# Optimization experiments

Measured on AMD Instinct MI355X. Metric: run time of the kernel, lower is better.

Reference implementation:

```python
import jax, jax.numpy as jnp
import numpy as np

N = 100000   # nodes
H = 96       # hidden_dim
A = 32       # attn_dim
De = 16      # edge_embeddings_dim
E = 500000   # edges per edge type
NEG_SLOPE = 0.01  # torch F.leaky_relu default


def setup_inputs() -> dict:
    key = jax.random.key(0)
    ks = jax.random.split(key, 24)
    nrm = lambda k, shape, s=1.0: jax.random.normal(k, shape, dtype=jnp.float32) * s
    idx = lambda k: jax.random.randint(k, (E,), 0, N, dtype=jnp.int32)
    Din = 2 * H + De
    return {
        'h': nrm(ks[0], (N, H)),
        'src0': idx(ks[1]), 'dst0': idx(ks[2]),
        'src1': idx(ks[3]), 'dst1': idx(ks[4]),
        'src2': idx(ks[5]), 'dst2': idx(ks[6]),
        'Wm0': nrm(ks[7], (Din, H), Din ** -0.5), 'bm0': jnp.zeros((H,), jnp.float32), 'ef0': nrm(ks[8], (De,)),
        'Wm1': nrm(ks[9], (Din, H), Din ** -0.5), 'bm1': jnp.zeros((H,), jnp.float32), 'ef1': nrm(ks[10], (De,)),
        'Wm2': nrm(ks[11], (Din, H), Din ** -0.5), 'bm2': jnp.zeros((H,), jnp.float32), 'ef2': nrm(ks[12], (De,)),
        'Wn0': nrm(ks[13], (H, A), H ** -0.5), 'Wa0': nrm(ks[14], (2 * A, 1), (2 * A) ** -0.5),
        'Wn1': nrm(ks[15], (H, A), H ** -0.5), 'Wa1': nrm(ks[16], (2 * A, 1), (2 * A) ** -0.5),
        'Wu': nrm(ks[17], (4 * H, H), (4 * H) ** -0.5), 'bu': jnp.zeros((H,), jnp.float32),
    }


def _leaky(x):
    return jnp.where(x > 0, x, NEG_SLOPE * x)


def _edge_msg(h, src, dst, Wm, bm, ef):
    # cat(src_h, dst_h, edge_feature) -> Linear  (dropout p=0, eval mode)
    x = jnp.concatenate([h[src], h[dst], jnp.broadcast_to(ef, (src.shape[0], ef.shape[0]))], axis=-1)
    return x @ Wm + bm  # [E, H]


def _mean_agg(m, dst):
    # fn.mean('m','msg'): per-destination mean over incoming edges
    s = jax.ops.segment_sum(m, dst, num_segments=N)
    c = jax.ops.segment_sum(jnp.ones((m.shape[0],), m.dtype), dst, num_segments=N)
    return s / jnp.maximum(c, 1.0)[:, None]


def _attn_agg(scores, m, dst):
    # per-destination softmax over mailbox (variable-size), then weighted sum
    smax = jax.ops.segment_max(scores, dst, num_segments=N)
    ex = jnp.exp(scores - smax[dst])
    den = jax.ops.segment_sum(ex, dst, num_segments=N)
    num = jax.ops.segment_sum(ex[:, None] * m, dst, num_segments=N)
    return num / jnp.maximum(den, 1e-9)[:, None]


def reference(h, src0, dst0, src1, dst1, src2, dst2,
              Wm0, bm0, ef0, Wm1, bm1, ef1, Wm2, bm2, ef2,
              Wn0, Wa0, Wn1, Wa1, Wu, bu):
    # edge type 0: intra_diff (attention), type 1: inter_diff (attention), type 2: intra_lt (mean)
    m0 = _edge_msg(h, src0, dst0, Wm0, bm0, ef0)
    m1 = _edge_msg(h, src1, dst1, Wm1, bm1, ef1)
    m2 = _edge_msg(h, src2, dst2, Wm2, bm2, ef2)

    z0 = h @ Wn0  # [N, A]
    s0 = _leaky(jnp.concatenate([z0[src0], z0[dst0]], axis=-1) @ Wa0)[:, 0]  # [E]
    z1 = h @ Wn1
    s1 = _leaky(jnp.concatenate([z1[src1], z1[dst1]], axis=-1) @ Wa1)[:, 0]

    msg0 = _attn_agg(s0, m0, dst0)   # [N, H]
    msg1 = _attn_agg(s1, m1, dst1)
    msg2 = _mean_agg(m2, dst2)

    # cross_reducer='stack' then concat over edge-type dim -> [N, 3H]
    mcat = jnp.concatenate([msg0, msg1, msg2], axis=-1)
    # cell node update: Linear(cat(h, m)) + ReLU
    return jax.nn.relu(jnp.concatenate([h, mcat], axis=-1) @ Wu + bu)
```

## Files before the change

kernel.cpp:

```cpp
#include <hip/hip_runtime.h>
#include <hip/hip_bf16.h>
#include <cstdint>

#define NN 100000
#define HH 96
#define AD 32
#define DE 16
#define EE 500000
#define NEG 0.01f

#define GSH 9
#define GSZ 512
#define KB 196
#define CH 2048
#define BPT 245
#define PCAP 801056

#define PREP_B 128
#define CAST_B 12500
#define HIST_B 512

typedef __bf16 bf16x8 __attribute__((ext_vector_type(8)));
typedef float  f32x4  __attribute__((ext_vector_type(4)));
typedef unsigned long long ull;
typedef unsigned long long ull2 __attribute__((ext_vector_type(2)));

__device__ __forceinline__ unsigned short f2b(float x) {
    union { float f; unsigned int u; } v; v.f = x;
    unsigned int r = v.u + 0x7fffu + ((v.u >> 16) & 1u);
    return (unsigned short)(r >> 16);
}
__device__ __forceinline__ float b2f(unsigned short h) {
    union { unsigned int u; float f; } v; v.u = ((unsigned int)h) << 16;
    return v.f;
}

__global__ __launch_bounds__(256) void setup_kernel(
    const float* __restrict__ h,
    const float* Wm0, const float* bm0, const float* ef0,
    const float* Wm1, const float* bm1, const float* ef1,
    const float* Wm2, const float* bm2, const float* ef2,
    const float* Wn0, const float* Wa0,
    const float* Wn1, const float* Wa1,
    const float* Wu,
    const int* __restrict__ d0, const int* __restrict__ d1,
    const int* __restrict__ d2,
    float* cvec, float* wvec,
    unsigned short* BfN, unsigned short* BfU,
    unsigned short* __restrict__ hb, float* __restrict__ uv,
    int* __restrict__ bCnt) {
    __shared__ int hist[3 * KB];
    int bid = blockIdx.x;
    int t = threadIdx.x;
    if (bid < PREP_B) {
        const float* Wm[3] = {Wm0, Wm1, Wm2};
        const float* bm[3] = {bm0, bm1, bm2};
        const float* ef[3] = {ef0, ef1, ef2};
        const int total = 288 + 384 + 55296 + 36864;
        for (int i = bid * 256 + t; i < total; i += PREP_B * 256) {
            if (i < 288) {
                int ty = i / 96, j = i % 96;
                float s = bm[ty][j];
                for (int k = 0; k < DE; ++k) s += ef[ty][k] * Wm[ty][(2 * HH + k) * HH + j];
                cvec[i] = s;
            } else if (i < 288 + 384) {
                int ii = i - 288;
                int kind = ii / 96, k = ii % 96;
                const float* Wn = (kind < 2) ? Wn0 : Wn1;
                const float* Wa = (kind < 2) ? Wa0 : Wa1;
                int off = (kind & 1) ? AD : 0;
                float s = 0.f;
                for (int a = 0; a < AD; ++a) s += Wn[k * AD + a] * Wa[off + a];
                wvec[ii] = s;
            } else if (i < 288 + 384 + 55296) {
                int ii = i - 672;
                int sec = ii / 9216; int rem = ii % 9216;
                int ksc = rem / 512; int lj = rem % 512;
                int ks = ksc / 6, c = ksc % 6;
                int lane = lj / 8, jj = lj % 8;
                int quad = lane / 16, m = lane % 16;
                int k = ks * 32 + quad * 8 + jj;
                int n = c * 16 + m;
                int mt = (sec < 3) ? sec : sec - 3;
                int rowoff = (sec < 3) ? 0 : HH;
                BfN[ii] = f2b(Wm[mt][(rowoff + k) * HH + n]);
            } else {
                int ii = i - (672 + 55296);
                int ksc = ii / 512; int lj = ii % 512;
                int ks = ksc / 6, c = ksc % 6;
                int lane = lj / 8, jj = lj % 8;
                int quad = lane / 16, m = lane % 16;
                int k = ks * 32 + quad * 8 + jj;
                int n = c * 16 + m;
                BfU[ii] = f2b(Wu[k * HH + n]);
            }
        }
    } else if (bid < PREP_B + CAST_B) {
        int lane = t & 31;
        int node = (((bid - PREP_B) * 256 + t) >> 5);
        if (node >= NN) return;
        float h0 = h[node * HH + lane];
        float h1 = h[node * HH + 32 + lane];
        float h2 = h[node * HH + 64 + lane];
        hb[node * HH + lane] = f2b(h0);
        hb[node * HH + 32 + lane] = f2b(h1);
        hb[node * HH + 64 + lane] = f2b(h2);
        float acc[4];
#pragma unroll
        for (int q = 0; q < 4; ++q)
            acc[q] = h0 * wvec[q * 96 + lane] + h1 * wvec[q * 96 + 32 + lane] +
                     h2 * wvec[q * 96 + 64 + lane];
#pragma unroll
        for (int d = 16; d >= 1; d >>= 1)
#pragma unroll
            for (int q = 0; q < 4; ++q) acc[q] += __shfl_down(acc[q], d, 32);
        if (lane == 0) {
#pragma unroll
            for (int q = 0; q < 4; ++q) uv[q * NN + node] = acc[q];
        }
    } else {
        int hb_ = bid - (PREP_B + CAST_B);
        for (int j = t; j < 3 * KB; j += 256) hist[j] = 0;
        __syncthreads();
        const int total = 3 * EE;
        for (int i = hb_ * 256 + t; i < total; i += HIST_B * 256) {
            int ty = i / EE, e = i - ty * EE;
            const int* d = (ty == 0) ? d0 : (ty == 1) ? d1 : d2;
            atomicAdd(&hist[ty * KB + (d[e] >> GSH)], 1);
        }
        __syncthreads();
        for (int j = t; j < 3 * KB; j += 256)
            if (hist[j]) atomicAdd(&bCnt[j], hist[j]);
    }
}

__global__ void cast_uv_fix_kernel(const float* __restrict__ h,
                                   const float* __restrict__ Wn0, const float* __restrict__ Wa0,
                                   const float* __restrict__ Wn1, const float* __restrict__ Wa1,
                                   float* __restrict__ uv) {
}

__global__ void bucket_scan(const int* __restrict__ bCnt, int* __restrict__ bBase,
                            int* __restrict__ gCursor) {
    __shared__ int hist[3 * KB];
    int t = threadIdx.x;
    if (t < 3 * KB) hist[t] = bCnt[t];
    __syncthreads();
    if (t < 3) {
        int run = 0;
        for (int b = 0; b < KB; ++b) {
            bBase[t * (KB + 1) + b] = run;
            gCursor[t * KB + b] = run;
            run += hist[t * KB + b];
        }
        bBase[t * (KB + 1) + KB] = run;
    }
}

__global__ __launch_bounds__(256) void bucket_scatter(
    const int* __restrict__ s0, const int* __restrict__ d0,
    const int* __restrict__ s1, const int* __restrict__ d1,
    const int* __restrict__ s2, const int* __restrict__ d2,
    int* __restrict__ gCursor, unsigned int* __restrict__ binned) {
    __shared__ unsigned int recs[CH];
    __shared__ unsigned short rnk[CH];
    __shared__ unsigned char bkt[CH];
    __shared__ int cnt[KB];
    __shared__ int gpos[KB];
    int t = threadIdx.x;
    int type = blockIdx.x / BPT;
    int chunk = (blockIdx.x % BPT) * CH;
    const int* src = (type == 0) ? s0 : (type == 1) ? s1 : s2;
    const int* dst = (type == 0) ? d0 : (type == 1) ? d1 : d2;
    if (t < KB) cnt[t] = 0;
    __syncthreads();
#pragma unroll
    for (int k = 0; k < CH / 256; ++k) {
        int idx = k * 256 + t;
        int e = chunk + idx;
        if (e < EE) {
            int s = src[e], d = dst[e];
            int b = d >> GSH;
            recs[idx] = ((unsigned int)s << GSH) | (unsigned int)(d & (GSZ - 1));
            bkt[idx] = (unsigned char)b;
            rnk[idx] = (unsigned short)atomicAdd(&cnt[b], 1);
        } else {
            bkt[idx] = 0xFF;
        }
    }
    __syncthreads();
    if (t < KB) {
        int c = cnt[t];
        gpos[t] = (c > 0) ? atomicAdd(&gCursor[type * KB + t], c) : 0;
    }
    __syncthreads();
    unsigned int* bout = binned + (size_t)type * EE;
#pragma unroll
    for (int k = 0; k < CH / 256; ++k) {
        int idx = k * 256 + t;
        unsigned char b = bkt[idx];
        if (b != 0xFF) bout[gpos[b] + rnk[idx]] = recs[idx];
    }
}

__global__ __launch_bounds__(256) void bucket_sort(
    const unsigned int* __restrict__ binned, const int* __restrict__ bBase,
    const float* __restrict__ uv,
    ull* __restrict__ rse, ull* __restrict__ wrec) {
    __shared__ int cnt[GSZ];
    __shared__ float vbuf[GSZ];
    __shared__ int wsum[4];
    int t = threadIdx.x;
    int type = blockIdx.x / KB;
    int b = blockIdx.x % KB;
    int nodeBase = b * GSZ;
    int eb = bBase[type * (KB + 1) + b];
    int en = bBase[type * (KB + 1) + b + 1];
    int n = en - eb;
    int pbase = eb + 3 * GSZ * b;
    const unsigned int* bin = binned + (size_t)type * EE + eb;
    cnt[t] = 0;
    cnt[t + 256] = 0;
    if (type < 2) {
        const float* vsrc = uv + (2 * type + 1) * NN;
        int nd0 = nodeBase + t, nd1 = nodeBase + 256 + t;
        vbuf[t] = (nd0 < NN) ? vsrc[nd0] : 0.f;
        vbuf[t + 256] = (nd1 < NN) ? vsrc[nd1] : 0.f;
    }
    __syncthreads();
    for (int i = t; i < n; i += 256) atomicAdd(&cnt[bin[i] & (GSZ - 1)], 1);
    __syncthreads();
    int v0 = cnt[t * 2], v1 = cnt[t * 2 + 1];
    int p0 = (v0 + 3) & ~3, p1 = (v1 + 3) & ~3;
    int s = p0 + p1;
    int lane = t & 63, wv = t >> 6;
    int val = s;
#pragma unroll
    for (int d = 1; d < 64; d <<= 1) {
        int o = __shfl_up(val, d, 64);
        if (lane >= d) val += o;
    }
    if (lane == 63) wsum[wv] = val;
    __syncthreads();
    int wpre = 0;
#pragma unroll
    for (int i = 0; i < 4; ++i) wpre += (i < wv) ? wsum[i] : 0;
    int excl = val - s + wpre;
    int off0 = excl, off1 = excl + p0;
    ull* wb = wrec + (size_t)type * PCAP;
    int node0 = nodeBase + t * 2, node1 = nodeBase + t * 2 + 1;
    if (node0 < NN) {
        rse[(size_t)type * NN + node0] =
            ((ull)(unsigned int)p0 << 32) | (unsigned int)(pbase + off0);
        for (int q = v0; q < p0; ++q) wb[pbase + off0 + q] = 0ull;
    }
    if (node1 < NN) {
        rse[(size_t)type * NN + node1] =
            ((ull)(unsigned int)p1 << 32) | (unsigned int)(pbase + off1);
        for (int q = v1; q < p1; ++q) wb[pbase + off1 + q] = 0ull;
    }
    __syncthreads();
    cnt[t * 2] = off0;
    cnt[t * 2 + 1] = off1;
    __syncthreads();
    const float* usrc = uv + 2 * type * NN;
    for (int i = t; i < n; i += 256) {
        unsigned int r = bin[i];
        int dl = r & (GSZ - 1);
        int p = atomicAdd(&cnt[dl], 1);
        unsigned int sidx = r >> GSH;
        float w = 1.f;
        if (type < 2) {
            float c = usrc[sidx] + vbuf[dl];
            c = fmaxf(c, NEG * c);
            w = __expf(c);
        }
        wb[pbase + p] = ((ull)__float_as_uint(w) << 32) | (ull)(sidx * 192u);
    }
}

__global__ void aggregate_kernel(const ull* __restrict__ rse,
                                 const ull* __restrict__ wrec,
                                 const unsigned short* __restrict__ hb,
                                 unsigned short* __restrict__ hagg,
                                 float* __restrict__ den) {
    const size_t NH = (size_t)NN * HH;
    int lane = threadIdx.x & 31;
    int node = (blockIdx.x * blockDim.x + threadIdx.x) >> 5;
    if (node >= NN) return;
    int t = blockIdx.y;
    ull se = rse[(size_t)t * NN + node];
    int beg = (int)(unsigned int)se;
    int end = beg + (int)(se >> 32);
    const ull* wr = wrec + (size_t)t * PCAP;
    float a0 = 0.f, a1 = 0.f, a2 = 0.f, dn = 0.f;
    const char* b0 = (const char*)hb + 4 * lane;
    const char* b1 = (const char*)hb + 128 + 2 * lane;
#define EDGE(rec)                                                              \
    {                                                                          \
        float w = __uint_as_float((unsigned int)((rec) >> 32));                \
        unsigned int off = (unsigned int)(rec);                                \
        unsigned int dv = *(const unsigned int*)(b0 + off);                    \
        unsigned int sv = *(const unsigned short*)(b1 + off);                  \
        a0 += w * __uint_as_float(dv << 16);                                   \
        a1 += w * __uint_as_float(dv & 0xFFFF0000u);                           \
        a2 += w * __uint_as_float(sv << 16);                                   \
        dn += w;                                                               \
    }
    for (int j = beg; j < end; j += 4) {
        ull2 p0 = *(const ull2*)(wr + j);
        ull2 p1 = *(const ull2*)(wr + j + 2);
        EDGE(p0[0]);
        EDGE(p0[1]);
        EDGE(p1[0]);
        EDGE(p1[1]);
    }
#undef EDGE
    float inv = (dn > 0.f) ? 1.f / dn : 0.f;
    float q0 = a0 * inv, q1 = a1 * inv, q2 = a2 * inv;
    char* mr = (char*)(hagg + (size_t)t * NH + (size_t)node * HH);
    *(unsigned int*)(mr + 4 * lane) =
        (unsigned int)f2b(q0) | ((unsigned int)f2b(q1) << 16);
    *(unsigned short*)(mr + 128 + 2 * lane) = f2b(q2);
    if (lane == 0) den[(size_t)t * NN + node] = dn;
}

__global__ __launch_bounds__(256) void msg_gemm_kernel(const unsigned short* __restrict__ hagg,
                                                       const unsigned short* __restrict__ hb,
                                                       const unsigned short* __restrict__ BfN,
                                                       const float* __restrict__ den,
                                                       const float* __restrict__ cvec,
                                                       unsigned short* __restrict__ msgb) {
    const size_t NH = (size_t)NN * HH;
    int wave = threadIdx.x >> 6;
    int lane = threadIdx.x & 63;
    int quad = lane >> 4, m = lane & 15;
    int blk = blockIdx.x * 4 + wave;
    if (blk >= NN / 16) return;
    int r0 = blk * 16;
    bf16x8 hf[3];
#pragma unroll
    for (int ks = 0; ks < 3; ++ks)
        hf[ks] = *(const bf16x8*)(hb + (size_t)(r0 + m) * HH + ks * 32 + quad * 8);
    for (int t = 0; t < 3; ++t) {
        const unsigned short* ha = hagg + (size_t)t * NH;
        f32x4 acc[6] = {};
#pragma unroll
        for (int ks = 0; ks < 3; ++ks) {
            bf16x8 af = *(const bf16x8*)(ha + (size_t)(r0 + m) * HH + ks * 32 + quad * 8);
#pragma unroll
            for (int c = 0; c < 6; ++c) {
                bf16x8 bfv = *(const bf16x8*)(BfN + (((t * 3 + ks) * 6 + c) << 9) + lane * 8);
                acc[c] = __builtin_amdgcn_mfma_f32_16x16x32_bf16(af, bfv, acc[c], 0, 0, 0);
            }
        }
#pragma unroll
        for (int ks = 0; ks < 3; ++ks) {
#pragma unroll
            for (int c = 0; c < 6; ++c) {
                bf16x8 bfv = *(const bf16x8*)(BfN + ((((t + 3) * 3 + ks) * 6 + c) << 9) + lane * 8);
                acc[c] = __builtin_amdgcn_mfma_f32_16x16x32_bf16(hf[ks], bfv, acc[c], 0, 0, 0);
            }
        }
        float dn[4];
#pragma unroll
        for (int r = 0; r < 4; ++r) dn[r] = den[(size_t)t * NN + r0 + quad * 4 + r];
#pragma unroll
        for (int c = 0; c < 6; ++c) {
            float cv = cvec[t * 96 + c * 16 + m];
#pragma unroll
            for (int r = 0; r < 4; ++r) {
                int row = r0 + quad * 4 + r;
                float val = (dn[r] > 0.f) ? (acc[c][r] + cv) : 0.f;
                msgb[(size_t)row * 288 + t * 96 + c * 16 + m] = f2b(val);
            }
        }
    }
}

__global__ __launch_bounds__(256) void update_gemm_kernel(const unsigned short* __restrict__ hb,
                                                          const unsigned short* __restrict__ msgb,
                                                          const unsigned short* __restrict__ BfU,
                                                          const float* __restrict__ bu,
                                                          float* __restrict__ out) {
    int wave = threadIdx.x >> 6;
    int lane = threadIdx.x & 63;
    int quad = lane >> 4, m = lane & 15;
    int blk = blockIdx.x * 4 + wave;
    if (blk >= NN / 16) return;
    int r0 = blk * 16;
    f32x4 acc[6] = {};
#pragma unroll
    for (int ks = 0; ks < 12; ++ks) {
        const unsigned short* ap =
            (ks < 3) ? hb + (size_t)(r0 + m) * HH + ks * 32 + quad * 8
                     : msgb + (size_t)(r0 + m) * 288 + (ks - 3) * 32 + quad * 8;
        bf16x8 af = *(const bf16x8*)ap;
#pragma unroll
        for (int c = 0; c < 6; ++c) {
            bf16x8 bfv = *(const bf16x8*)(BfU + ((ks * 6 + c) << 9) + lane * 8);
            acc[c] = __builtin_amdgcn_mfma_f32_16x16x32_bf16(af, bfv, acc[c], 0, 0, 0);
        }
    }
#pragma unroll
    for (int c = 0; c < 6; ++c) {
        float b = bu[c * 16 + m];
#pragma unroll
        for (int r = 0; r < 4; ++r) {
            int row = r0 + quad * 4 + r;
            float v2 = acc[c][r] + b;
            out[(size_t)row * HH + c * 16 + m] = v2 > 0.f ? v2 : 0.f;
        }
    }
}

extern "C" void kernel_launch(void* const* d_in, const int* in_sizes, int n_in,
                              void* d_out, int out_size, void* d_ws, size_t ws_size,
                              hipStream_t stream) {
    (void)in_sizes; (void)n_in; (void)out_size;
    const float* h   = (const float*)d_in[0];
    const int* srcs[3] = {(const int*)d_in[1], (const int*)d_in[3], (const int*)d_in[5]};
    const int* dsts[3] = {(const int*)d_in[2], (const int*)d_in[4], (const int*)d_in[6]};
    const float* Wm0 = (const float*)d_in[7];
    const float* bm0 = (const float*)d_in[8];
    const float* ef0 = (const float*)d_in[9];
    const float* Wm1 = (const float*)d_in[10];
    const float* bm1 = (const float*)d_in[11];
    const float* ef1 = (const float*)d_in[12];
    const float* Wm2 = (const float*)d_in[13];
    const float* bm2 = (const float*)d_in[14];
    const float* ef2 = (const float*)d_in[15];
    const float* Wn0 = (const float*)d_in[16];
    const float* Wa0 = (const float*)d_in[17];
    const float* Wn1 = (const float*)d_in[18];
    const float* Wa1 = (const float*)d_in[19];
    const float* Wu  = (const float*)d_in[20];
    const float* bu  = (const float*)d_in[21];
    float* out = (float*)d_out;

    const size_t NEED = 165019776;
    if (ws_size < NEED) return;
    char* w = (char*)d_ws;
    unsigned short* msgb    = (unsigned short*)(w + 0);
    unsigned short* hb      = (unsigned short*)(w + 57600000);
    unsigned short* hagg    = (unsigned short*)(w + 76800000);
    float*          den     = (float*)(w + 134400000);
    float*          uv      = (float*)(w + 135600000);
    float*          cvec    = (float*)(w + 137200000);
    float*          wvec    = (float*)(w + 137201280);
    unsigned short* BfN     = (unsigned short*)(w + 137202816);
    unsigned short* BfU     = (unsigned short*)(w + 137313408);
    int*            bBase   = (int*)(w + 137387136);
    int*            gCursor = (int*)(w + 137389568);
    int*            bCnt    = (int*)(w + 137392000);
    ull*            rse     = (ull*)(w + 137394432);
    unsigned int*   binned  = (unsigned int*)(w + 139794432);
    ull*            wrec    = (ull*)(w + 145794432);

    hipMemsetAsync(bCnt, 0, 3 * KB * sizeof(int), stream);
    {
        struct L {
            static __global__ void k(const float* Wn0, const float* Wa0,
                                     const float* Wn1, const float* Wa1,
                                     float* wvec) {
                int ii = blockIdx.x * 192 + threadIdx.x;
                if (ii >= 384) return;
                int kind = ii / 96, kk = ii % 96;
                const float* Wn = (kind < 2) ? Wn0 : Wn1;
                const float* Wa = (kind < 2) ? Wa0 : Wa1;
                int off = (kind & 1) ? AD : 0;
                float s = 0.f;
                for (int a = 0; a < AD; ++a) s += Wn[kk * AD + a] * Wa[off + a];
                wvec[ii] = s;
            }
        };
        L::k<<<2, 192, 0, stream>>>(Wn0, Wa0, Wn1, Wa1, wvec);
    }
    setup_kernel<<<PREP_B + CAST_B + HIST_B, 256, 0, stream>>>(
        h, Wm0, bm0, ef0, Wm1, bm1, ef1, Wm2, bm2, ef2,
        Wn0, Wa0, Wn1, Wa1, Wu, dsts[0], dsts[1], dsts[2],
        cvec, wvec, BfN, BfU, hb, uv, bCnt);
    bucket_scan<<<1, 640, 0, stream>>>(bCnt, bBase, gCursor);
    bucket_scatter<<<3 * BPT, 256, 0, stream>>>(srcs[0], dsts[0], srcs[1], dsts[1],
                                                srcs[2], dsts[2], gCursor, binned);
    bucket_sort<<<3 * KB, 256, 0, stream>>>(binned, bBase, uv, rse, wrec);

    aggregate_kernel<<<dim3(12500, 3), 256, 0, stream>>>(rse, wrec, hb, hagg, den);
    msg_gemm_kernel<<<1563, 256, 0, stream>>>(hagg, hb, BfN, den, cvec, msgb);
    update_gemm_kernel<<<1563, 256, 0, stream>>>(hb, msgb, BfU, bu, out);
}
```

Before: 327.4 us.

## Fold message linear into update weights and fuse the two output GEMMs

Precomputes combined weights Wm·Wu so the per-edge-type message projection and the node-update GEMM run as one 384-wide GEMM directly on aggregated features. This removes the intermediate bf16 message buffer and a whole kernel. Nodes with no incoming edges of some type get their spurious constant and dst-term contributions subtracted in a new fixup kernel using a stored correction matrix. The trade-off is heavier serial weight precompute in setup, with per-thread 96-long dot products, plus an extra pass over the output. The folded bf16 weights may also lose some precision.

```diff
diff --git a/kernel.cpp b/kernel.cpp
--- a/kernel.cpp
+++ b/kernel.cpp
@@ -40,13 +40,11 @@
     const float* Wm0, const float* bm0, const float* ef0,
     const float* Wm1, const float* bm1, const float* ef1,
     const float* Wm2, const float* bm2, const float* ef2,
-    const float* Wn0, const float* Wa0,
-    const float* Wn1, const float* Wa1,
     const float* Wu,
     const int* __restrict__ d0, const int* __restrict__ d1,
     const int* __restrict__ d2,
-    float* cvec, float* wvec,
-    unsigned short* BfN, unsigned short* BfU,
+    const float* __restrict__ wvec,
+    unsigned short* BfF, float* Dmat, float* cb,
     unsigned short* __restrict__ hb, float* __restrict__ uv,
     int* __restrict__ bCnt) {
     __shared__ int hist[3 * KB];
@@ -56,43 +54,55 @@
         const float* Wm[3] = {Wm0, Wm1, Wm2};
         const float* bm[3] = {bm0, bm1, bm2};
         const float* ef[3] = {ef0, ef1, ef2};
-        const int total = 288 + 384 + 55296 + 36864;
+        const int T_BFF = 36864, T_D = 27648, T_CB = 288;
+        const int total = T_BFF + T_D + T_CB;
         for (int i = bid * 256 + t; i < total; i += PREP_B * 256) {
-            if (i < 288) {
-                int ty = i / 96, j = i % 96;
-                float s = bm[ty][j];
-                for (int k = 0; k < DE; ++k) s += ef[ty][k] * Wm[ty][(2 * HH + k) * HH + j];
-                cvec[i] = s;
-            } else if (i < 288 + 384) {
-                int ii = i - 288;
-                int kind = ii / 96, k = ii % 96;
-                const float* Wn = (kind < 2) ? Wn0 : Wn1;
-                const float* Wa = (kind < 2) ? Wa0 : Wa1;
-                int off = (kind & 1) ? AD : 0;
-                float s = 0.f;
-                for (int a = 0; a < AD; ++a) s += Wn[k * AD + a] * Wa[off + a];
-                wvec[ii] = s;
-            } else if (i < 288 + 384 + 55296) {
-                int ii = i - 672;
-                int sec = ii / 9216; int rem = ii % 9216;
-                int ksc = rem / 512; int lj = rem % 512;
+            if (i < T_BFF) {
+                int ksc = i / 512, lj = i % 512;
                 int ks = ksc / 6, c = ksc % 6;
                 int lane = lj / 8, jj = lj % 8;
                 int quad = lane / 16, m = lane % 16;
                 int k = ks * 32 + quad * 8 + jj;
                 int n = c * 16 + m;
-                int mt = (sec < 3) ? sec : sec - 3;
-                int rowoff = (sec < 3) ? 0 : HH;
-                BfN[ii] = f2b(Wm[mt][(rowoff + k) * HH + n]);
+                float s;
+                if (k < 96) {
+                    s = Wu[k * HH + n];
+                    for (int tt = 0; tt < 3; ++tt) {
+                        const float* wm = Wm[tt];
+                        float a = 0.f;
+                        for (int j = 0; j < 96; ++j)
+                            a += wm[(96 + k) * HH + j] * Wu[(96 + 96 * tt + j) * HH + n];
+                        s += a;
+                    }
+                } else {
+                    int tt = (k - 96) / 96, kk = (k - 96) % 96;
+                    const float* wm = Wm[tt];
+                    s = 0.f;
+                    for (int j = 0; j < 96; ++j)
+                        s += wm[kk * HH + j] * Wu[(96 + 96 * tt + j) * HH + n];
+                }
+                BfF[i] = f2b(s);
+            } else if (i < T_BFF + T_D) {
+                int ii = i - T_BFF;
+                int tt = ii / 9216, r = ii % 9216;
+                int k = r / 96, n = r % 96;
+                const float* wm = Wm[tt];
+                float s = 0.f;
+                for (int j = 0; j < 96; ++j)
+                    s += wm[(96 + k) * HH + j] * Wu[(96 + 96 * tt + j) * HH + n];
+                Dmat[ii] = s;
             } else {
-                int ii = i - (672 + 55296);
-                int ksc = ii / 512; int lj = ii % 512;
-                int ks = ksc / 6, c = ksc % 6;
-                int lane = lj / 8, jj = lj % 8;
-                int quad = lane / 16, m = lane % 16;
-                int k = ks * 32 + quad * 8 + jj;
-                int n = c * 16 + m;
-                BfU[ii] = f2b(Wu[k * HH + n]);
+                int ii = i - T_BFF - T_D;
+                int tt = ii / 96, n = ii % 96;
+                const float* wm = Wm[tt];
+                float s = 0.f;
+                for (int k = 0; k < 96; ++k) {
+                    float cv = bm[tt][k];
+                    for (int j = 0; j < DE; ++j)
+                        cv += ef[tt][j] * wm[(192 + j) * HH + k];
+                    s += cv * Wu[(96 + 96 * tt + k) * HH + n];
+                }
+                cb[ii] = s;
             }
         }
     } else if (bid < PREP_B + CAST_B) {
@@ -132,12 +142,6 @@
         for (int j = t; j < 3 * KB; j += 256)
             if (hist[j]) atomicAdd(&bCnt[j], hist[j]);
     }
-}
-
-__global__ void cast_uv_fix_kernel(const float* __restrict__ h,
-                                   const float* __restrict__ Wn0, const float* __restrict__ Wa0,
-                                   const float* __restrict__ Wn1, const float* __restrict__ Wa1,
-                                   float* __restrict__ uv) {
 }
 
 __global__ void bucket_scan(const int* __restrict__ bCnt, int* __restrict__ bBase,
@@ -325,12 +329,14 @@
     if (lane == 0) den[(size_t)t * NN + node] = dn;
 }
 
-__global__ __launch_bounds__(256) void msg_gemm_kernel(const unsigned short* __restrict__ hagg,
-                                                       const unsigned short* __restrict__ hb,
-                                                       const unsigned short* __restrict__ BfN,
-                                                       const float* __restrict__ den,
-                                                       const float* __restrict__ cvec,
-                                                       unsigned short* __restrict__ msgb) {
+__global__ __launch_bounds__(256) void fused_out_kernel(
+    const unsigned short* __restrict__ hagg,
+    const unsigned short* __restrict__ hb,
+    const unsigned short* __restrict__ BfF,
+    const float* __restrict__ den,
+    const float* __restrict__ cb,
+    const float* __restrict__ bu,
+    float* __restrict__ out) {
     const size_t NH = (size_t)NN * HH;
     int wave = threadIdx.x >> 6;
     int lane = threadIdx.x & 63;
@@ -338,79 +344,80 @@
     int blk = blockIdx.x * 4 + wave;
     if (blk >= NN / 16) return;
     int r0 = blk * 16;
-    bf16x8 hf[3];
-#pragma unroll
-    for (int ks = 0; ks < 3; ++ks)
-        hf[ks] = *(const bf16x8*)(hb + (size_t)(r0 + m) * HH + ks * 32 + quad * 8);
-    for (int t = 0; t < 3; ++t) {
-        const unsigned short* ha = hagg + (size_t)t * NH;
-        f32x4 acc[6] = {};
-#pragma unroll
-        for (int ks = 0; ks < 3; ++ks) {
-            bf16x8 af = *(const bf16x8*)(ha + (size_t)(r0 + m) * HH + ks * 32 + quad * 8);
-#pragma unroll
-            for (int c = 0; c < 6; ++c) {
-                bf16x8 bfv = *(const bf16x8*)(BfN + (((t * 3 + ks) * 6 + c) << 9) + lane * 8);
-                acc[c] = __builtin_amdgcn_mfma_f32_16x16x32_bf16(af, bfv, acc[c], 0, 0, 0);
-            }
-        }
-#pragma unroll
-        for (int ks = 0; ks < 3; ++ks) {
-#pragma unroll
-            for (int c = 0; c < 6; ++c) {
-                bf16x8 bfv = *(const bf16x8*)(BfN + ((((t + 3) * 3 + ks) * 6 + c) << 9) + lane * 8);
-                acc[c] = __builtin_amdgcn_mfma_f32_16x16x32_bf16(hf[ks], bfv, acc[c], 0, 0, 0);
-            }
-        }
-        float dn[4];
-#pragma unroll
-        for (int r = 0; r < 4; ++r) dn[r] = den[(size_t)t * NN + r0 + quad * 4 + r];
-#pragma unroll
-        for (int c = 0; c < 6; ++c) {
-            float cv = cvec[t * 96 + c * 16 + m];
-#pragma unroll
-            for (int r = 0; r < 4; ++r) {
-                int row = r0 + quad * 4 + r;
-                float val = (dn[r] > 0.f) ? (acc[c][r] + cv) : 0.f;
-                msgb[(size_t)row * 288 + t * 96 + c * 16 + m] = f2b(val);
-            }
-        }
-    }
-}
-
-__global__ __launch_bounds__(256) void update_gemm_kernel(const unsigned short* __restrict__ hb,
-                                                          const unsigned short* __restrict__ msgb,
-                                                          const unsigned short* __restrict__ BfU,
-                                                          const float* __restrict__ bu,
-                                                          float* __restrict__ out) {
-    int wave = threadIdx.x >> 6;
-    int lane = threadIdx.x & 63;
-    int quad = lane >> 4, m = lane & 15;
-    int blk = blockIdx.x * 4 + wave;
-    if (blk >= NN / 16) return;
-    int r0 = blk * 16;
     f32x4 acc[6] = {};
 #pragma unroll
     for (int ks = 0; ks < 12; ++ks) {
         const unsigned short* ap =
             (ks < 3) ? hb + (size_t)(r0 + m) * HH + ks * 32 + quad * 8
-                     : msgb + (size_t)(r0 + m) * 288 + (ks - 3) * 32 + quad * 8;
+                     : hagg + (size_t)((ks - 3) / 3) * NH + (size_t)(r0 + m) * HH +
+                           ((ks - 3) % 3) * 32 + quad * 8;
         bf16x8 af = *(const bf16x8*)ap;
 #pragma unroll
         for (int c = 0; c < 6; ++c) {
-            bf16x8 bfv = *(const bf16x8*)(BfU + ((ks * 6 + c) << 9) + lane * 8);
+            bf16x8 bfv = *(const bf16x8*)(BfF + ((ks * 6 + c) << 9) + lane * 8);
             acc[c] = __builtin_amdgcn_mfma_f32_16x16x32_bf16(af, bfv, acc[c], 0, 0, 0);
         }
     }
+    float dn0[4], dn1[4], dn2[4];
+#pragma unroll
+    for (int r = 0; r < 4; ++r) {
+        int row = r0 + quad * 4 + r;
+        dn0[r] = den[row];
+        dn1[r] = den[NN + row];
+        dn2[r] = den[2 * NN + row];
+    }
 #pragma unroll
     for (int c = 0; c < 6; ++c) {
-        float b = bu[c * 16 + m];
+        int n = c * 16 + m;
+        float bias = bu[n] + cb[n] + cb[96 + n] + cb[192 + n];
 #pragma unroll
         for (int r = 0; r < 4; ++r) {
             int row = r0 + quad * 4 + r;
-            float v2 = acc[c][r] + b;
-            out[(size_t)row * HH + c * 16 + m] = v2 > 0.f ? v2 : 0.f;
-        }
+            float v = acc[c][r] + bias;
+            bool clean = (dn0[r] > 0.f) && (dn1[r] > 0.f) && (dn2[r] > 0.f);
+            out[(size_t)row * HH + n] = clean ? (v > 0.f ? v : 0.f) : v;
+        }
+    }
+}
+
+__global__ __launch_bounds__(256) void fixup_kernel(
+    const float* __restrict__ den,
+    const unsigned short* __restrict__ hb,
+    const float* __restrict__ Dmat,
+    const float* __restrict__ cb,
+    float* __restrict__ out) {
+    int lane = threadIdx.x & 31;
+    int group = (blockIdx.x * 256 + threadIdx.x) >> 5;
+    int ngroups = (gridDim.x * 256) >> 5;
+    for (int node = group; node < NN; node += ngroups) {
+        float d0 = den[node], d1 = den[NN + node], d2 = den[2 * NN + node];
+        bool z0 = !(d0 > 0.f), z1 = !(d1 > 0.f), z2 = !(d2 > 0.f);
+        if (!(z0 | z1 | z2)) continue;
+        const unsigned short* hr = hb + (size_t)node * HH;
+        float c0 = 0.f, c1 = 0.f, c2 = 0.f;
+#pragma unroll 1
+        for (int tt = 0; tt < 3; ++tt) {
+            bool z = (tt == 0) ? z0 : (tt == 1) ? z1 : z2;
+            if (!z) continue;
+            const float* D = Dmat + tt * 9216;
+            float a0 = cb[tt * 96 + lane];
+            float a1 = cb[tt * 96 + 32 + lane];
+            float a2 = cb[tt * 96 + 64 + lane];
+            for (int k = 0; k < 96; ++k) {
+                float hv = b2f(hr[k]);
+                a0 += hv * D[k * 96 + lane];
+                a1 += hv * D[k * 96 + 32 + lane];
+                a2 += hv * D[k * 96 + 64 + lane];
+            }
+            c0 += a0; c1 += a1; c2 += a2;
+        }
+        float* orow = out + (size_t)node * HH;
+        float v0 = orow[lane] - c0;
+        float v1 = orow[32 + lane] - c1;
+        float v2 = orow[64 + lane] - c2;
+        orow[lane] = v0 > 0.f ? v0 : 0.f;
+        orow[32 + lane] = v1 > 0.f ? v1 : 0.f;
+        orow[64 + lane] = v2 > 0.f ? v2 : 0.f;
     }
 }
 
@@ -438,24 +445,23 @@
     const float* bu  = (const float*)d_in[21];
     float* out = (float*)d_out;
 
-    const size_t NEED = 165019776;
+    const size_t NEED = 107419648;
     if (ws_size < NEED) return;
     char* w = (char*)d_ws;
-    unsigned short* msgb    = (unsigned short*)(w + 0);
-    unsigned short* hb      = (unsigned short*)(w + 57600000);
-    unsigned short* hagg    = (unsigned short*)(w + 76800000);
-    float*          den     = (float*)(w + 134400000);
-    float*          uv      = (float*)(w + 135600000);
-    float*          cvec    = (float*)(w + 137200000);
-    float*          wvec    = (float*)(w + 137201280);
-    unsigned short* BfN     = (unsigned short*)(w + 137202816);
-    unsigned short* BfU     = (unsigned short*)(w + 137313408);
-    int*            bBase   = (int*)(w + 137387136);
-    int*            gCursor = (int*)(w + 137389568);
-    int*            bCnt    = (int*)(w + 137392000);
-    ull*            rse     = (ull*)(w + 137394432);
-    unsigned int*   binned  = (unsigned int*)(w + 139794432);
-    ull*            wrec    = (ull*)(w + 145794432);
+    unsigned short* hb      = (unsigned short*)(w + 0);
+    unsigned short* hagg    = (unsigned short*)(w + 19200000);
+    float*          den     = (float*)(w + 76800000);
+    float*          uv      = (float*)(w + 78000000);
+    float*          wvec    = (float*)(w + 79600000);
+    unsigned short* BfF     = (unsigned short*)(w + 79601536);
+    float*          Dmat    = (float*)(w + 79675264);
+    float*          cb      = (float*)(w + 79785856);
+    int*            bBase   = (int*)(w + 79787008);
+    int*            gCursor = (int*)(w + 79789440);
+    int*            bCnt    = (int*)(w + 79791872);
+    ull*            rse     = (ull*)(w + 79794304);
+    unsigned int*   binned  = (unsigned int*)(w + 82194304);
+    ull*            wrec    = (ull*)(w + 88194304);
 
     hipMemsetAsync(bCnt, 0, 3 * KB * sizeof(int), stream);
     {
@@ -477,15 +483,14 @@
         L::k<<<2, 192, 0, stream>>>(Wn0, Wa0, Wn1, Wa1, wvec);
     }
     setup_kernel<<<PREP_B + CAST_B + HIST_B, 256, 0, stream>>>(
-        h, Wm0, bm0, ef0, Wm1, bm1, ef1, Wm2, bm2, ef2,
-        Wn0, Wa0, Wn1, Wa1, Wu, dsts[0], dsts[1], dsts[2],
-        cvec, wvec, BfN, BfU, hb, uv, bCnt);
+        h, Wm0, bm0, ef0, Wm1, bm1, ef1, Wm2, bm2, ef2, Wu,
+        dsts[0], dsts[1], dsts[2], wvec, BfF, Dmat, cb, hb, uv, bCnt);
     bucket_scan<<<1, 640, 0, stream>>>(bCnt, bBase, gCursor);
     bucket_scatter<<<3 * BPT, 256, 0, stream>>>(srcs[0], dsts[0], srcs[1], dsts[1],
                                                 srcs[2], dsts[2], gCursor, binned);
     bucket_sort<<<3 * KB, 256, 0, stream>>>(binned, bBase, uv, rse, wrec);
 
     aggregate_kernel<<<dim3(12500, 3), 256, 0, stream>>>(rse, wrec, hb, hagg, den);
-    msg_gemm_kernel<<<1563, 256, 0, stream>>>(hagg, hb, BfN, den, cvec, msgb);
-    update_gemm_kernel<<<1563, 256, 0, stream>>>(hb, msgb, BfU, bu, out);
-}
+    fused_out_kernel<<<1563, 256, 0, stream>>>(hagg, hb, BfF, den, cb, bu, out);
+    fixup_kernel<<<784, 256, 0, stream>>>(den, hb, Dmat, cb, out);
+}
```

New measurement: 326.9 us. No clear change (-0.1%).
